# Kernel optimization log

Measured on AMD Instinct MI355X. Metric: run time of the kernel, lower is better.

## Reference

```python
import jax, jax.numpy as jnp
import numpy as np

EPS = 1e-8       # slot-attention eps
LN_EPS = 1e-5    # torch LayerNorm default
ITERS = 3        # num_iterations


def _ln(x, g, b):
    m = jnp.mean(x, axis=-1, keepdims=True)
    v = jnp.var(x, axis=-1, keepdims=True)
    return (x - m) * jax.lax.rsqrt(v + LN_EPS) * g + b


def setup_inputs() -> dict:
    key = jax.random.key(0)
    ks = jax.random.split(key, 16)
    B, N, S, D = 64, 4096, 8, 256
    s = 1.0 / np.sqrt(D)
    inp = {}
    inp["inputs"] = jax.random.normal(ks[0], (B, N, D), jnp.float32)
    inp["init_slots"] = jax.random.normal(ks[1], (B, S, D), jnp.float32)
    inp["wq"] = jax.random.normal(ks[2], (D, D), jnp.float32) * s
    inp["bq"] = jnp.zeros((D,), jnp.float32)
    inp["wk"] = jax.random.normal(ks[3], (D, D), jnp.float32) * s
    inp["bk"] = jnp.zeros((D,), jnp.float32)
    inp["wv"] = jax.random.normal(ks[4], (D, D), jnp.float32) * s
    inp["bv"] = jnp.zeros((D,), jnp.float32)
    inp["w_ih"] = jax.random.normal(ks[5], (3 * D, D), jnp.float32) * s
    inp["b_ih"] = jnp.zeros((3 * D,), jnp.float32)
    inp["w_hh"] = jax.random.normal(ks[6], (3 * D, D), jnp.float32) * s
    inp["b_hh"] = jnp.zeros((3 * D,), jnp.float32)
    inp["w1"] = jax.random.normal(ks[7], (D, D), jnp.float32) * s  # fc1_slot (hidden_dim == D)
    inp["b1"] = jnp.zeros((D,), jnp.float32)
    inp["w2"] = jax.random.normal(ks[8], (D, D), jnp.float32) * s  # fc2_slot
    inp["b2"] = jnp.zeros((D,), jnp.float32)
    inp["g_in"] = jnp.ones((D,), jnp.float32)
    inp["b_in"] = jnp.zeros((D,), jnp.float32)
    inp["g_slots"] = jnp.ones((D,), jnp.float32)
    inp["b_slots"] = jnp.zeros((D,), jnp.float32)
    inp["g_ff"] = jnp.ones((D,), jnp.float32)
    inp["b_ff"] = jnp.zeros((D,), jnp.float32)
    return inp


def reference(inputs, init_slots, wq, bq, wk, bk, wv, bv, w_ih, b_ih, w_hh, b_hh,
              w1, b1, w2, b2, g_in, b_in, g_slots, b_slots, g_ff, b_ff):
    D = inputs.shape[-1]
    scale = D ** (-0.5)
    # img_k_v: LayerNorm inputs, project to k, v
    x = _ln(inputs, g_in, b_in)
    k = x @ wk.T + bk  # [B,N,D]
    v = x @ wv.T + bv  # [B,N,D]
    slots = init_slots  # [B,S,D]
    for _ in range(ITERS):
        prev = slots
        sn = _ln(slots, g_slots, b_slots)
        q = sn @ wq.T + bq                                   # [B,S,D]
        dots = jnp.einsum('bid,bjd->bij', q, k) * scale      # [B,S,N]
        attn = jax.nn.softmax(dots, axis=1) + EPS            # softmax over slots
        attn = attn / jnp.sum(attn, axis=-1, keepdims=True)  # normalize over inputs
        updates = jnp.einsum('bjd,bij->bid', v, attn)        # [B,S,D]
        # GRUCell(updates, prev): torch gate ordering r, z, n
        gx = updates @ w_ih.T + b_ih
        gh = prev @ w_hh.T + b_hh
        xr, xz, xn = jnp.split(gx, 3, axis=-1)
        hr, hz, hn = jnp.split(gh, 3, axis=-1)
        r = jax.nn.sigmoid(xr + hr)
        z = jax.nn.sigmoid(xz + hz)
        n = jnp.tanh(xn + r * hn)
        slots = (1.0 - z) * n + z * prev
        # residual MLP
        h = jax.nn.relu(_ln(slots, g_ff, b_ff) @ w1.T + b1)
        slots = slots + h @ w2.T + b2
    return slots
```

## Files before the change

kernel.cpp:

```cpp
#include <hip/hip_runtime.h>
#include <hip/hip_bf16.h>
#include <stdint.h>

typedef unsigned short u16;
typedef __attribute__((ext_vector_type(8))) short short8;
typedef __attribute__((ext_vector_type(4))) float f32x4;

#define NB 64
#define NN 4096
#define NS 8
#define ND 256
#define NSEG 16
#define GROWS (NB*NN)

__device__ inline u16 f2bf(float f) {
    uint32_t u = __float_as_uint(f);
    u = (u + 0x7FFFu + ((u >> 16) & 1u)) >> 16;
    return (u16)u;
}
__device__ inline float bf2f(u16 h) {
    return __uint_as_float(((uint32_t)h) << 16);
}
__device__ inline f32x4 mfma16(short8 a, short8 b, f32x4 c) {
    return __builtin_amdgcn_mfma_f32_16x16x32_bf16(a, b, c, 0, 0, 0);
}
__device__ inline void gload_lds16(const u16* g, u16* l) {
    __builtin_amdgcn_global_load_lds(
        (const __attribute__((address_space(1))) void*)g,
        (__attribute__((address_space(3))) void*)l,
        16, 0, 0);
}

__global__ __launch_bounds__(256) void prep_w(
        const float* __restrict__ wv, const float* __restrict__ wk, const float* __restrict__ wq,
        const float* __restrict__ wih, const float* __restrict__ whh,
        const float* __restrict__ w1, const float* __restrict__ w2,
        u16* __restrict__ wvb, u16* __restrict__ wkTb, u16* __restrict__ wqTb,
        u16* __restrict__ wihb, u16* __restrict__ whhb,
        u16* __restrict__ w1b, u16* __restrict__ w2b) {
    int i = blockIdx.x * 256 + threadIdx.x;
    if (i < 65536) { wvb[i] = f2bf(wv[i]); return; }
    i -= 65536;
    if (i < 65536) { wkTb[i] = f2bf(wk[(i & 255)*256 + (i >> 8)]); return; }
    i -= 65536;
    if (i < 65536) { wqTb[i] = f2bf(wq[(i & 255)*256 + (i >> 8)]); return; }
    i -= 65536;
    if (i < 196608) { wihb[i] = f2bf(wih[i]); return; }
    i -= 196608;
    if (i < 196608) { whhb[i] = f2bf(whh[i]); return; }
    i -= 196608;
    if (i < 65536) { w1b[i] = f2bf(w1[i]); return; }
    i -= 65536;
    if (i < 65536) w2b[i] = f2bf(w2[i]);
}

__global__ __launch_bounds__(256) void prep_M(
        const u16* __restrict__ wkTb, const u16* __restrict__ wqTb, u16* __restrict__ Mb,
        const float* __restrict__ wq, const float* __restrict__ bk, float* __restrict__ uvec) {
    if (blockIdx.x == 16) {
        int m = threadIdx.x;
        float acc = 0.f;
        for (int o = 0; o < 256; o++) acc += wq[o*256 + m] * bk[o];
        uvec[m] = acc;
        return;
    }
    const int d0 = blockIdx.x * 16;
    const int tid = threadIdx.x, wid = tid >> 6, lane = tid & 63;
    const int l15 = lane & 15, quad = lane >> 4, kq = quad * 8;
    short8 af[8];
#pragma unroll
    for (int k = 0; k < 8; k++)
        af[k] = *reinterpret_cast<const short8*>(&wkTb[(size_t)(d0 + l15)*256 + k*32 + kq]);
#pragma unroll
    for (int ct = 0; ct < 4; ct++) {
        int m0 = (wid*4 + ct)*16;
        f32x4 a = (f32x4){0.f,0.f,0.f,0.f};
#pragma unroll
        for (int k = 0; k < 8; k++) {
            short8 bw = *reinterpret_cast<const short8*>(&wqTb[(size_t)(m0 + l15)*256 + k*32 + kq]);
            a = mfma16(af[k], bw, a);
        }
#pragma unroll
        for (int r = 0; r < 4; r++)
            Mb[(size_t)(d0 + quad*4 + r)*256 + m0 + l15] = f2bf(a[r]);
    }
}

__global__ __launch_bounds__(256) void ln_cast(
        const float* __restrict__ inp, const float* __restrict__ g,
        const float* __restrict__ bt, u16* __restrict__ xb) {
    const int tid = threadIdx.x, wid = tid >> 6, lane = tid & 63;
    const long r0 = (long)blockIdx.x * 64 + wid * 16;
    float4 g4 = reinterpret_cast<const float4*>(g)[lane];
    float4 b4 = reinterpret_cast<const float4*>(bt)[lane];
#pragma unroll 4
    for (int i = 0; i < 16; i++) {
        long row = r0 + i;
        float4 v = reinterpret_cast<const float4*>(inp + row*256)[lane];
        float s = v.x + v.y + v.z + v.w;
        float ss = v.x*v.x + v.y*v.y + v.z*v.z + v.w*v.w;
#pragma unroll
        for (int off = 32; off >= 1; off >>= 1) { s += __shfl_xor(s, off, 64); ss += __shfl_xor(ss, off, 64); }
        float mean = s * (1.0f/256.0f);
        float rstd = rsqrtf(ss * (1.0f/256.0f) - mean*mean + 1e-5f);
        ushort4 o;
        o.x = f2bf((v.x-mean)*rstd*g4.x + b4.x);
        o.y = f2bf((v.y-mean)*rstd*g4.y + b4.y);
        o.z = f2bf((v.z-mean)*rstd*g4.z + b4.z);
        o.w = f2bf((v.w-mean)*rstd*g4.w + b4.w);
        reinterpret_cast<ushort4*>(xb + row*256)[lane] = o;
    }
}

__global__ __launch_bounds__(256) void q_proj(
        const float* __restrict__ slots, const u16* __restrict__ Mb,
        const float* __restrict__ uvec,
        const float* __restrict__ gs, const float* __restrict__ bs,
        u16* __restrict__ qb, float* __restrict__ cvec) {
    __shared__ u16 sn[16*264];
    const int b = blockIdx.x;
    const int tid = threadIdx.x, wid = tid >> 6, lane = tid & 63;
    const int l15 = lane & 15, kq = (lane >> 4) * 8;
    for (int rr = wid; rr < 8; rr += 4) {
        float4 v = reinterpret_cast<const float4*>(slots + (size_t)(b*8 + rr)*256)[lane];
        float s = v.x + v.y + v.z + v.w;
        float ss = v.x*v.x + v.y*v.y + v.z*v.z + v.w*v.w;
#pragma unroll
        for (int off = 32; off >= 1; off >>= 1) { s += __shfl_xor(s, off, 64); ss += __shfl_xor(ss, off, 64); }
        float mean = s * (1.f/256.f);
        float rstd = rsqrtf(ss * (1.f/256.f) - mean*mean + 1e-5f);
        float4 g4 = reinterpret_cast<const float4*>(gs)[lane];
        float4 b4 = reinterpret_cast<const float4*>(bs)[lane];
        ushort4 o;
        o.x = f2bf((v.x-mean)*rstd*g4.x + b4.x);
        o.y = f2bf((v.y-mean)*rstd*g4.y + b4.y);
        o.z = f2bf((v.z-mean)*rstd*g4.z + b4.z);
        o.w = f2bf((v.w-mean)*rstd*g4.w + b4.w);
        *reinterpret_cast<ushort4*>(&sn[rr*264 + lane*4]) = o;
    }
    {
        ushort4 z = {0,0,0,0};
        for (int rr = 8 + wid; rr < 16; rr += 4)
            *reinterpret_cast<ushort4*>(&sn[rr*264 + lane*4]) = z;
    }
    __syncthreads();
    {
        int s = tid >> 5, l = tid & 31;
        float p = 0.f;
#pragma unroll
        for (int i = 0; i < 8; i++)
            p += bf2f(sn[s*264 + l*8 + i]) * uvec[l*8 + i];
#pragma unroll
        for (int off = 16; off >= 1; off >>= 1) p += __shfl_xor(p, off, 64);
        if (l == 0) cvec[b*8 + s] = p;
    }
    short8 af[8];
#pragma unroll
    for (int k = 0; k < 8; k++) af[k] = *reinterpret_cast<const short8*>(&sn[l15*264 + k*32 + kq]);
#pragma unroll
    for (int ct = 0; ct < 4; ct++) {
        int o0 = (wid*4 + ct)*16;
        f32x4 a = (f32x4){0.f,0.f,0.f,0.f};
#pragma unroll
        for (int k = 0; k < 8; k++) {
            short8 bw = *reinterpret_cast<const short8*>(&Mb[(size_t)(o0 + l15)*256 + k*32 + kq]);
            a = mfma16(af[k], bw, a);
        }
        if (lane < 32) {
            int sb = (lane >> 4)*4;
#pragma unroll
            for (int r = 0; r < 4; r++)
                qb[(size_t)(b*8 + sb + r)*256 + o0 + l15] = f2bf(a[r]);
        }
    }
}

__global__ __launch_bounds__(256) void attn(
        const u16* __restrict__ qt, const u16* __restrict__ xrow,
        const float* __restrict__ cvec,
        float* __restrict__ num_part, float* __restrict__ den_part) {
    __shared__ u16 xt[4][32*256];
    __shared__ u16 pb_all[4][16*36];
    __shared__ float dpd[4][8];
    const int b = blockIdx.x >> 4;
    const int seg = blockIdx.x & 15;
    const int tid = threadIdx.x, wid = tid >> 6, lane = tid & 63;
    const int l15 = lane & 15, quad = lane >> 4, kq = quad * 8;
    u16* xw = xt[wid];
    u16* pb = pb_all[wid];
    const int n_w = seg*256 + wid*64;

    {
        const int half = lane >> 5, c = lane & 31;
#pragma unroll
        for (int i = 0; i < 16; i++) {
            const int r = i*2 + half;
            const int key = (r & 7) ^ ((r >> 3) << 1);
            gload_lds16(xrow + (size_t)(b*4096 + n_w + r)*256 + (c ^ key)*8, &xw[i*2*256]);
        }
    }
#pragma unroll
    for (int k2 = 0; k2 < 9; k2++) pb[lane + k2*64] = 0;

    short8 aq[8];
    {
        const u16* qrow = &qt[((size_t)b*8 + (l15 & 7))*256 + kq];
        short8 z = {0,0,0,0,0,0,0,0};
#pragma unroll
        for (int kk = 0; kk < 8; kk++) {
            short8 t = *reinterpret_cast<const short8*>(&qrow[kk*32]);
            aq[kk] = (l15 < 8) ? t : z;
        }
    }
    float cc[4];
#pragma unroll
    for (int r = 0; r < 4; r++) {
        int rowi = quad*4 + r;
        cc[r] = (rowi < 8) ? cvec[b*8 + rowi] : 0.f;
    }
    f32x4 acc[16];
#pragma unroll
    for (int dt = 0; dt < 16; dt++) acc[dt] = (f32x4){0.f,0.f,0.f,0.f};
    float psum[4] = {0.f,0.f,0.f,0.f};

    for (int ch = 0; ch < 2; ch++) {
        const int nc = n_w + ch*32;
        const u16* kbase = &xrow[((size_t)b*4096 + nc + l15)*256 + kq];
        short8 kf[8], kn[8];
#pragma unroll
        for (int kk = 0; kk < 8; kk++) kf[kk] = *reinterpret_cast<const short8*>(&kbase[kk*32]);
#pragma unroll
        for (int nt = 0; nt < 2; nt++) {
            f32x4 dd = (f32x4){0.f,0.f,0.f,0.f};
            if (nt == 0) {
#pragma unroll
                for (int kk = 0; kk < 8; kk++) dd = mfma16(aq[kk], kf[kk], dd);
                const u16* kp = kbase + (size_t)16*256;
#pragma unroll
                for (int kk = 0; kk < 8; kk++) kn[kk] = *reinterpret_cast<const short8*>(&kp[kk*32]);
            } else {
#pragma unroll
                for (int kk = 0; kk < 8; kk++) dd = mfma16(aq[kk], kn[kk], dd);
            }
            float t0 = (dd[0] + cc[0])*0.0625f, t1 = (dd[1] + cc[1])*0.0625f;
            float t2 = (dd[2] + cc[2])*0.0625f, t3 = (dd[3] + cc[3])*0.0625f;
            float m4 = fmaxf(fmaxf(t0,t1), fmaxf(t2,t3));
            float m8 = fmaxf(m4, __shfl_xor(m4, 16, 64));
            float e0 = __expf(t0-m8), e1 = __expf(t1-m8), e2 = __expf(t2-m8), e3 = __expf(t3-m8);
            float s4 = e0+e1+e2+e3;
            float s8 = s4 + __shfl_xor(s4, 16, 64);
            float inv = 1.0f / s8;
            u16 h0 = f2bf(e0*inv + 1e-8f);
            u16 h1 = f2bf(e1*inv + 1e-8f);
            u16 h2 = f2bf(e2*inv + 1e-8f);
            u16 h3 = f2bf(e3*inv + 1e-8f);
            if (lane < 32) {
                int sb = quad*4, col = nt*16 + l15;
                pb[(sb+0)*36 + col] = h0;
                pb[(sb+1)*36 + col] = h1;
                pb[(sb+2)*36 + col] = h2;
                pb[(sb+3)*36 + col] = h3;
                psum[0] += bf2f(h0); psum[1] += bf2f(h1);
                psum[2] += bf2f(h2); psum[3] += bf2f(h3);
            }
        }
        __builtin_amdgcn_s_waitcnt(0x0070);
        __builtin_amdgcn_sched_barrier(0);
        short8 ap = *reinterpret_cast<const short8*>(&pb[l15*36 + kq]);
        const int d = l15;
#pragma unroll
        for (int dt = 0; dt < 16; dt++) {
            const int dd2 = dt*16 + d;
            const int d3 = dd2 >> 3, d7 = dd2 & 7;
            const int rowb = quad*8*256 + d7;
            const int c3 = d3 ^ (quad << 1);
            short8 pv;
#pragma unroll
            for (int j = 0; j < 8; j++)
                pv[j] = (short)xw[rowb + j*256 + ((c3 ^ j) << 3)];
            acc[dt] = mfma16(ap, pv, acc[dt]);
        }
        if (ch == 0) {
            const int half = lane >> 5, c = lane & 31;
#pragma unroll
            for (int i = 0; i < 16; i++) {
                const int r = i*2 + half;
                const int key = (r & 7) ^ ((r >> 3) << 1);
                gload_lds16(xrow + (size_t)(b*4096 + n_w + 32 + r)*256 + (c ^ key)*8, &xw[i*2*256]);
            }
        }
    }
#pragma unroll
    for (int off = 1; off < 16; off <<= 1) {
#pragma unroll
        for (int r = 0; r < 4; r++) psum[r] += __shfl_xor(psum[r], off, 64);
    }
    if (quad < 2 && l15 == 0) {
#pragma unroll
        for (int r = 0; r < 4; r++) dpd[wid][quad*4 + r] = psum[r];
    }
    float* rw = (float*)&xt[wid][0];
    if (lane < 32) {
        int sb = quad*4;
#pragma unroll
        for (int dt = 0; dt < 16; dt++) {
            int d0 = dt*16 + l15;
#pragma unroll
            for (int r = 0; r < 4; r++)
                rw[(sb+r)*256 + d0] = acc[dt][r];
        }
    }
    __syncthreads();
    const float* F = (const float*)&xt[0][0];
    for (int idx = tid; idx < 2048; idx += 256) {
        float v = F[idx] + F[4096 + idx] + F[8192 + idx] + F[12288 + idx];
        num_part[((size_t)(b*16 + seg))*2048 + idx] = v;
    }
    if (tid < 8)
        den_part[(b*16 + seg)*8 + tid] = dpd[0][tid] + dpd[1][tid] + dpd[2][tid] + dpd[3][tid];
}

__global__ __launch_bounds__(768) void finalize(
        const float* __restrict__ slots_in, const float* __restrict__ num_part, const float* __restrict__ den_part,
        const u16* __restrict__ wihb, const float* __restrict__ bih,
        const u16* __restrict__ whhb, const float* __restrict__ bhh,
        const u16* __restrict__ w1b, const float* __restrict__ b1v,
        const u16* __restrict__ w2b, const float* __restrict__ b2v,
        const u16* __restrict__ wvb, const float* __restrict__ bvv,
        const float* __restrict__ gff, const float* __restrict__ bff,
        float* __restrict__ slots_out,
        const u16* __restrict__ Mb, const float* __restrict__ uvec,
        const float* __restrict__ gs, const float* __restrict__ bs,
        u16* __restrict__ qb, float* __restrict__ cvec, int do_q) {
    __shared__ u16 updb[16*264];
    __shared__ u16 prevb[16*264];
    __shared__ u16 lnb[16*264];
    __shared__ float gx[8*776];
    __shared__ float gh[8*776];
    __shared__ float snew[8*256];
    __shared__ float dsum_s[8];
    float* sfin = gx;
    const int b = blockIdx.x;
    const int tid = threadIdx.x, wid = tid >> 6, lane = tid & 63;
    const int l15 = lane & 15, kq = (lane >> 4) * 8;
    if (tid < 8) {
        float ds = 0.f;
#pragma unroll
        for (int sg = 0; sg < 16; sg++) ds += den_part[(b*16 + sg)*8 + tid];
        dsum_s[tid] = ds;
    }
    __syncthreads();
    for (int idx = tid; idx < 2048; idx += 768) {
        int s = idx >> 8, d = idx & 255;
        float ns = 0.f;
#pragma unroll
        for (int sg = 0; sg < 16; sg++)
            ns += num_part[((size_t)(b*16 + sg)*8 + s)*256 + d];
        updb[s*264 + d] = f2bf(ns / dsum_s[s]);
        prevb[s*264 + d] = f2bf(slots_in[(size_t)(b*8 + s)*256 + d]);
        updb[(8+s)*264 + d] = 0;
        prevb[(8+s)*264 + d] = 0;
        lnb[(8+s)*264 + d] = 0;
    }
    __syncthreads();
    {
        short8 av[8];
#pragma unroll
        for (int k = 0; k < 8; k++)
            av[k] = *reinterpret_cast<const short8*>(&updb[l15*264 + k*32 + kq]);
        for (int ct = wid; ct < 16; ct += 12) {
            int o0 = ct*16;
            f32x4 a = (f32x4){0.f,0.f,0.f,0.f};
#pragma unroll
            for (int k = 0; k < 8; k++) {
                short8 bw = *reinterpret_cast<const short8*>(&wvb[(size_t)(o0 + l15)*256 + k*32 + kq]);
                a = mfma16(av[k], bw, a);
            }
            if (lane < 32) {
                int sb = (lane >> 4)*4, o = o0 + l15;
                float bb2 = bvv[o];
#pragma unroll
                for (int r = 0; r < 4; r++)
                    lnb[(sb+r)*264 + o] = f2bf(a[r] + bb2);
            }
        }
    }
    __syncthreads();
    short8 au[8], ap[8];
#pragma unroll
    for (int k = 0; k < 8; k++) {
        au[k] = *reinterpret_cast<const short8*>(&lnb[l15*264 + k*32 + kq]);
        ap[k] = *reinterpret_cast<const short8*>(&prevb[l15*264 + k*32 + kq]);
    }
#pragma unroll
    for (int ct = 0; ct < 4; ct++) {
        int o0 = (wid*4 + ct)*16;
        f32x4 ax = (f32x4){0.f,0.f,0.f,0.f}, ah = (f32x4){0.f,0.f,0.f,0.f};
#pragma unroll
        for (int k = 0; k < 8; k++) {
            short8 bx = *reinterpret_cast<const short8*>(&wihb[(size_t)(o0 + l15)*256 + k*32 + kq]);
            short8 bh = *reinterpret_cast<const short8*>(&whhb[(size_t)(o0 + l15)*256 + k*32 + kq]);
            ax = mfma16(au[k], bx, ax);
            ah = mfma16(ap[k], bh, ah);
        }
        if (lane < 32) {
            int sb = (lane >> 4)*4, o = o0 + l15;
            float bxs = bih[o], bhs = bhh[o];
#pragma unroll
            for (int r = 0; r < 4; r++) {
                gx[(sb+r)*776 + o] = ax[r] + bxs;
                gh[(sb+r)*776 + o] = ah[r] + bhs;
            }
        }
    }
    __syncthreads();
    for (int idx = tid; idx < 2048; idx += 768) {
        int s = idx >> 8, j = idx & 255;
        float xr = gx[s*776 + j], xz = gx[s*776 + 256 + j], xn = gx[s*776 + 512 + j];
        float hr = gh[s*776 + j], hz = gh[s*776 + 256 + j], hn = gh[s*776 + 512 + j];
        float r_ = 1.f/(1.f + __expf(-(xr+hr)));
        float z_ = 1.f/(1.f + __expf(-(xz+hz)));
        float n_ = tanhf(xn + r_*hn);
        float pv = slots_in[(size_t)(b*8 + s)*256 + j];
        snew[s*256 + j] = (1.f - z_)*n_ + z_*pv;
    }
    __syncthreads();
    if (wid < 8) {
        int rr = wid;
        float4 v = reinterpret_cast<const float4*>(&snew[rr*256])[lane];
        float s = v.x + v.y + v.z + v.w;
        float ss = v.x*v.x + v.y*v.y + v.z*v.z + v.w*v.w;
#pragma unroll
        for (int off = 32; off >= 1; off >>= 1) { s += __shfl_xor(s, off, 64); ss += __shfl_xor(ss, off, 64); }
        float mean = s * (1.f/256.f);
        float rstd = rsqrtf(ss * (1.f/256.f) - mean*mean + 1e-5f);
        float4 g4 = reinterpret_cast<const float4*>(gff)[lane];
        float4 b4 = reinterpret_cast<const float4*>(bff)[lane];
        ushort4 o;
        o.x = f2bf((v.x-mean)*rstd*g4.x + b4.x);
        o.y = f2bf((v.y-mean)*rstd*g4.y + b4.y);
        o.z = f2bf((v.z-mean)*rstd*g4.z + b4.z);
        o.w = f2bf((v.w-mean)*rstd*g4.w + b4.w);
        *reinterpret_cast<ushort4*>(&lnb[rr*264 + lane*4]) = o;
    } else {
        ushort4 z = {0,0,0,0};
        *reinterpret_cast<ushort4*>(&lnb[wid*264 + lane*4]) = z;
        *reinterpret_cast<ushort4*>(&lnb[(wid+4)*264 + lane*4]) = z;
    }
    __syncthreads();
    short8 al[8];
#pragma unroll
    for (int k = 0; k < 8; k++) al[k] = *reinterpret_cast<const short8*>(&lnb[l15*264 + k*32 + kq]);
    for (int ct = wid; ct < 16; ct += 12) {
        int o0 = ct*16;
        f32x4 a = (f32x4){0.f,0.f,0.f,0.f};
#pragma unroll
        for (int k = 0; k < 8; k++) {
            short8 bw = *reinterpret_cast<const short8*>(&w1b[(size_t)(o0 + l15)*256 + k*32 + kq]);
            a = mfma16(al[k], bw, a);
        }
        if (lane < 32) {
            int sb = (lane >> 4)*4, o = o0 + l15;
            float bb = b1v[o];
#pragma unroll
            for (int r = 0; r < 4; r++)
                updb[(sb+r)*264 + o] = f2bf(fmaxf(a[r] + bb, 0.f));
        }
    }
    __syncthreads();
    short8 ah2[8];
#pragma unroll
    for (int k = 0; k < 8; k++) ah2[k] = *reinterpret_cast<const short8*>(&updb[l15*264 + k*32 + kq]);
    for (int ct = wid; ct < 16; ct += 12) {
        int o0 = ct*16;
        f32x4 a = (f32x4){0.f,0.f,0.f,0.f};
#pragma unroll
        for (int k = 0; k < 8; k++) {
            short8 bw = *reinterpret_cast<const short8*>(&w2b[(size_t)(o0 + l15)*256 + k*32 + kq]);
            a = mfma16(ah2[k], bw, a);
        }
        if (lane < 32) {
            int sb = (lane >> 4)*4, o = o0 + l15;
            float bb = b2v[o];
#pragma unroll
            for (int r = 0; r < 4; r++) {
                float vfin = snew[(sb+r)*256 + o] + a[r] + bb;
                slots_out[(size_t)(b*8 + sb + r)*256 + o] = vfin;
                sfin[(sb+r)*256 + o] = vfin;
            }
        }
    }
    if (!do_q) return;
    __syncthreads();
    if (wid < 8) {
        int rr = wid;
        float4 v = reinterpret_cast<const float4*>(&sfin[rr*256])[lane];
        float s = v.x + v.y + v.z + v.w;
        float ss = v.x*v.x + v.y*v.y + v.z*v.z + v.w*v.w;
#pragma unroll
        for (int off = 32; off >= 1; off >>= 1) { s += __shfl_xor(s, off, 64); ss += __shfl_xor(ss, off, 64); }
        float mean = s * (1.f/256.f);
        float rstd = rsqrtf(ss * (1.f/256.f) - mean*mean + 1e-5f);
        float4 g4 = reinterpret_cast<const float4*>(gs)[lane];
        float4 b4 = reinterpret_cast<const float4*>(bs)[lane];
        ushort4 o;
        o.x = f2bf((v.x-mean)*rstd*g4.x + b4.x);
        o.y = f2bf((v.y-mean)*rstd*g4.y + b4.y);
        o.z = f2bf((v.z-mean)*rstd*g4.z + b4.z);
        o.w = f2bf((v.w-mean)*rstd*g4.w + b4.w);
        *reinterpret_cast<ushort4*>(&lnb[rr*264 + lane*4]) = o;
    } else {
        ushort4 z = {0,0,0,0};
        *reinterpret_cast<ushort4*>(&lnb[wid*264 + lane*4]) = z;
        *reinterpret_cast<ushort4*>(&lnb[(wid+4)*264 + lane*4]) = z;
    }
    __syncthreads();
    if (tid < 256) {
        int s = tid >> 5, l = tid & 31;
        float p = 0.f;
#pragma unroll
        for (int i = 0; i < 8; i++)
            p += bf2f(lnb[s*264 + l*8 + i]) * uvec[l*8 + i];
#pragma unroll
        for (int off = 16; off >= 1; off >>= 1) p += __shfl_xor(p, off, 64);
        if (l == 0) cvec[b*8 + s] = p;
    }
    short8 alq[8];
#pragma unroll
    for (int k = 0; k < 8; k++) alq[k] = *reinterpret_cast<const short8*>(&lnb[l15*264 + k*32 + kq]);
    for (int ct = wid; ct < 16; ct += 12) {
        int o0 = ct*16;
        f32x4 a = (f32x4){0.f,0.f,0.f,0.f};
#pragma unroll
        for (int k = 0; k < 8; k++) {
            short8 bw = *reinterpret_cast<const short8*>(&Mb[(size_t)(o0 + l15)*256 + k*32 + kq]);
            a = mfma16(alq[k], bw, a);
        }
        if (lane < 32) {
            int sb = (lane >> 4)*4, o = o0 + l15;
#pragma unroll
            for (int r = 0; r < 4; r++)
                qb[(size_t)(b*8 + sb + r)*256 + o] = f2bf(a[r]);
        }
    }
}

extern "C" void kernel_launch(void* const* d_in, const int* in_sizes, int n_in,
                              void* d_out, int out_size, void* d_ws, size_t ws_size,
                              hipStream_t stream) {
    (void)in_sizes; (void)n_in; (void)out_size;
    const float* inputs     = (const float*)d_in[0];
    const float* init_slots = (const float*)d_in[1];
    const float* wq  = (const float*)d_in[2];
    const float* bq  = (const float*)d_in[3];  (void)bq;
    const float* wk  = (const float*)d_in[4];
    const float* bk  = (const float*)d_in[5];
    const float* wv  = (const float*)d_in[6];
    const float* bv  = (const float*)d_in[7];
    const float* wih = (const float*)d_in[8];
    const float* bih = (const float*)d_in[9];
    const float* whh = (const float*)d_in[10];
    const float* bhh = (const float*)d_in[11];
    const float* w1  = (const float*)d_in[12];
    const float* b1  = (const float*)d_in[13];
    const float* w2  = (const float*)d_in[14];
    const float* b2  = (const float*)d_in[15];
    const float* g_in = (const float*)d_in[16];
    const float* b_in = (const float*)d_in[17];
    const float* g_sl = (const float*)d_in[18];
    const float* b_sl = (const float*)d_in[19];
    const float* g_ff = (const float*)d_in[20];
    const float* b_ff = (const float*)d_in[21];

    char* ws = (char*)d_ws;
    size_t off = 0;
    auto alloc = [&](size_t bytes) -> void* {
        void* p = ws + off;
        off += (bytes + 255) & ~(size_t)255;
        return p;
    };
    u16* xb    = (u16*)alloc((size_t)GROWS * ND * 2);
    u16* qbf   = (u16*)alloc((size_t)NB * NS * ND * 2);
    float* slots = (float*)alloc((size_t)NB * NS * ND * 4);
    float* nump  = (float*)alloc((size_t)NB * NSEG * NS * ND * 4);
    float* denp  = (float*)alloc((size_t)NB * NSEG * NS * 4);
    float* cvec  = (float*)alloc((size_t)NB * NS * 4);
    float* uvec  = (float*)alloc(256 * 4);
    u16* wvb  = (u16*)alloc(65536 * 2);
    u16* wkTb = (u16*)alloc(65536 * 2);
    u16* wqTb = (u16*)alloc(65536 * 2);
    u16* Mb   = (u16*)alloc(65536 * 2);
    u16* wihb = (u16*)alloc(196608 * 2);
    u16* whhb = (u16*)alloc(196608 * 2);
    u16* w1b  = (u16*)alloc(65536 * 2);
    u16* w2b  = (u16*)alloc(65536 * 2);
    if (off > ws_size) return;

    prep_w<<<2816, 256, 0, stream>>>(wv, wk, wq, wih, whh, w1, w2,
                                     wvb, wkTb, wqTb, wihb, whhb, w1b, w2b);
    prep_M<<<17, 256, 0, stream>>>(wkTb, wqTb, Mb, wq, bk, uvec);
    hipMemcpyAsync(slots, init_slots, (size_t)NB * NS * ND * 4,
                   hipMemcpyDeviceToDevice, stream);
    ln_cast<<<GROWS / 64, 256, 0, stream>>>(inputs, g_in, b_in, xb);
    q_proj<<<NB, 256, 0, stream>>>(slots, Mb, uvec, g_sl, b_sl, qbf, cvec);
    for (int it = 0; it < 3; it++) {
        attn<<<NB * 16, 256, 0, stream>>>(qbf, xb, cvec, nump, denp);
        float* outp = (it == 2) ? (float*)d_out : slots;
        finalize<<<NB, 768, 0, stream>>>(slots, nump, denp, wihb, bih, whhb, bhh,
                                         w1b, b1, w2b, b2, wvb, bv, g_ff, b_ff, outp,
                                         Mb, uvec, g_sl, b_sl, qbf, cvec, (it < 2) ? 1 : 0);
    }
}
```

Baseline: 719.4 us.

## Restructure attn kernel into block-wide double-buffered 64-row tiles split by D

```diff
diff --git a/kernel.cpp b/kernel.cpp
--- a/kernel.cpp
+++ b/kernel.cpp
@@ -10,7 +10,7 @@
 #define NN 4096
 #define NS 8
 #define ND 256
-#define NSEG 16
+#define NSEG 8
 #define GROWS (NB*NN)
 
 __device__ inline u16 f2bf(float f) {
@@ -179,29 +179,34 @@
         const u16* __restrict__ qt, const u16* __restrict__ xrow,
         const float* __restrict__ cvec,
         float* __restrict__ num_part, float* __restrict__ den_part) {
-    __shared__ u16 xt[4][32*256];
-    __shared__ u16 pb_all[4][16*36];
+    __shared__ u16 xt[2][64*256];
+    __shared__ u16 pt[16*72];
     __shared__ float dpd[4][8];
-    const int b = blockIdx.x >> 4;
-    const int seg = blockIdx.x & 15;
+    const int b = blockIdx.x >> 3;
+    const int seg = blockIdx.x & 7;
     const int tid = threadIdx.x, wid = tid >> 6, lane = tid & 63;
     const int l15 = lane & 15, quad = lane >> 4, kq = quad * 8;
-    u16* xw = xt[wid];
-    u16* pb = pb_all[wid];
-    const int n_w = seg*256 + wid*64;
-
+    const int n0 = seg * 512;
+    const u16* xsrc = xrow + (size_t)b*4096*256;
+
+    auto STAGE = [&](int t) {
+        u16* dst = &xt[t & 1][(wid*16) * 256];
+        const u16* src = xsrc + (size_t)(n0 + t*64 + wid*16) * 256;
+        const int half = lane >> 5, c = lane & 31;
+#pragma unroll
+        for (int i = 0; i < 8; i++) {
+            const int rl = wid*16 + i*2 + half;
+            const int key = (rl & 7) ^ ((rl >> 3) & 7);
+            gload_lds16(src + (size_t)(i*2 + half)*256 + ((c ^ key))*8, dst + i*2*256);
+        }
+    };
+
+    STAGE(0);
     {
-        const int half = lane >> 5, c = lane & 31;
-#pragma unroll
-        for (int i = 0; i < 16; i++) {
-            const int r = i*2 + half;
-            const int key = (r & 7) ^ ((r >> 3) << 1);
-            gload_lds16(xrow + (size_t)(b*4096 + n_w + r)*256 + (c ^ key)*8, &xw[i*2*256]);
-        }
-    }
-#pragma unroll
-    for (int k2 = 0; k2 < 9; k2++) pb[lane + k2*64] = 0;
-
+        ushort4 z4 = {0,0,0,0};
+        if (tid < 144)
+            *reinterpret_cast<ushort4*>(&pt[8*72 + tid*4]) = z4;
+    }
     short8 aq[8];
     {
         const u16* qrow = &qt[((size_t)b*8 + (l15 & 7))*256 + kq];
@@ -218,77 +223,67 @@
         int rowi = quad*4 + r;
         cc[r] = (rowi < 8) ? cvec[b*8 + rowi] : 0.f;
     }
-    f32x4 acc[16];
-#pragma unroll
-    for (int dt = 0; dt < 16; dt++) acc[dt] = (f32x4){0.f,0.f,0.f,0.f};
+    f32x4 acc[4];
+#pragma unroll
+    for (int dt = 0; dt < 4; dt++) acc[dt] = (f32x4){0.f,0.f,0.f,0.f};
     float psum[4] = {0.f,0.f,0.f,0.f};
 
-    for (int ch = 0; ch < 2; ch++) {
-        const int nc = n_w + ch*32;
-        const u16* kbase = &xrow[((size_t)b*4096 + nc + l15)*256 + kq];
-        short8 kf[8], kn[8];
-#pragma unroll
-        for (int kk = 0; kk < 8; kk++) kf[kk] = *reinterpret_cast<const short8*>(&kbase[kk*32]);
-#pragma unroll
-        for (int nt = 0; nt < 2; nt++) {
-            f32x4 dd = (f32x4){0.f,0.f,0.f,0.f};
-            if (nt == 0) {
-#pragma unroll
-                for (int kk = 0; kk < 8; kk++) dd = mfma16(aq[kk], kf[kk], dd);
-                const u16* kp = kbase + (size_t)16*256;
-#pragma unroll
-                for (int kk = 0; kk < 8; kk++) kn[kk] = *reinterpret_cast<const short8*>(&kp[kk*32]);
-            } else {
-#pragma unroll
-                for (int kk = 0; kk < 8; kk++) dd = mfma16(aq[kk], kn[kk], dd);
+    __syncthreads();
+
+    for (int t = 0; t < 8; t++) {
+        if (t < 7) STAGE(t + 1);
+        const u16* tw = xt[t & 1];
+        const int rq = wid*16 + l15;
+        const int keyq = (rq & 7) ^ ((rq >> 3) & 7);
+        f32x4 dd = (f32x4){0.f,0.f,0.f,0.f};
+#pragma unroll
+        for (int kk = 0; kk < 8; kk++) {
+            short8 bf = *reinterpret_cast<const short8*>(
+                &tw[rq*256 + (((kk*4 + quad) ^ keyq))*8]);
+            dd = mfma16(aq[kk], bf, dd);
+        }
+        float t0 = (dd[0] + cc[0])*0.0625f, t1 = (dd[1] + cc[1])*0.0625f;
+        float t2 = (dd[2] + cc[2])*0.0625f, t3 = (dd[3] + cc[3])*0.0625f;
+        float m4 = fmaxf(fmaxf(t0,t1), fmaxf(t2,t3));
+        float m8 = fmaxf(m4, __shfl_xor(m4, 16, 64));
+        float e0 = __expf(t0-m8), e1 = __expf(t1-m8), e2 = __expf(t2-m8), e3 = __expf(t3-m8);
+        float s4 = e0+e1+e2+e3;
+        float s8 = s4 + __shfl_xor(s4, 16, 64);
+        float inv = 1.0f / s8;
+        u16 h0 = f2bf(e0*inv + 1e-8f);
+        u16 h1 = f2bf(e1*inv + 1e-8f);
+        u16 h2 = f2bf(e2*inv + 1e-8f);
+        u16 h3 = f2bf(e3*inv + 1e-8f);
+        if (lane < 32) {
+            int sb = quad*4, col = wid*16 + l15;
+            pt[(sb+0)*72 + col] = h0;
+            pt[(sb+1)*72 + col] = h1;
+            pt[(sb+2)*72 + col] = h2;
+            pt[(sb+3)*72 + col] = h3;
+            psum[0] += bf2f(h0); psum[1] += bf2f(h1);
+            psum[2] += bf2f(h2); psum[3] += bf2f(h3);
+        }
+        __syncthreads();
+        short8 ap0 = *reinterpret_cast<const short8*>(&pt[l15*72 + kq]);
+        short8 ap1 = *reinterpret_cast<const short8*>(&pt[l15*72 + 32 + kq]);
+#pragma unroll
+        for (int dt = 0; dt < 4; dt++) {
+            const int d = (wid*4 + dt)*16 + l15;
+            const int g = d >> 3, e = d & 7;
+            short8 pv0, pv1;
+#pragma unroll
+            for (int j = 0; j < 8; j++) {
+                const int ra = quad*8 + j;
+                const int ka = (ra & 7) ^ ((ra >> 3) & 7);
+                pv0[j] = (short)tw[ra*256 + ((g ^ ka))*8 + e];
+                const int rb2 = 32 + quad*8 + j;
+                const int kb2 = (rb2 & 7) ^ ((rb2 >> 3) & 7);
+                pv1[j] = (short)tw[rb2*256 + ((g ^ kb2))*8 + e];
             }
-            float t0 = (dd[0] + cc[0])*0.0625f, t1 = (dd[1] + cc[1])*0.0625f;
-            float t2 = (dd[2] + cc[2])*0.0625f, t3 = (dd[3] + cc[3])*0.0625f;
-            float m4 = fmaxf(fmaxf(t0,t1), fmaxf(t2,t3));
-            float m8 = fmaxf(m4, __shfl_xor(m4, 16, 64));
-            float e0 = __expf(t0-m8), e1 = __expf(t1-m8), e2 = __expf(t2-m8), e3 = __expf(t3-m8);
-            float s4 = e0+e1+e2+e3;
-            float s8 = s4 + __shfl_xor(s4, 16, 64);
-            float inv = 1.0f / s8;
-            u16 h0 = f2bf(e0*inv + 1e-8f);
-            u16 h1 = f2bf(e1*inv + 1e-8f);
-            u16 h2 = f2bf(e2*inv + 1e-8f);
-            u16 h3 = f2bf(e3*inv + 1e-8f);
-            if (lane < 32) {
-                int sb = quad*4, col = nt*16 + l15;
-                pb[(sb+0)*36 + col] = h0;
-                pb[(sb+1)*36 + col] = h1;
-                pb[(sb+2)*36 + col] = h2;
-                pb[(sb+3)*36 + col] = h3;
-                psum[0] += bf2f(h0); psum[1] += bf2f(h1);
-                psum[2] += bf2f(h2); psum[3] += bf2f(h3);
-            }
-        }
-        __builtin_amdgcn_s_waitcnt(0x0070);
-        __builtin_amdgcn_sched_barrier(0);
-        short8 ap = *reinterpret_cast<const short8*>(&pb[l15*36 + kq]);
-        const int d = l15;
-#pragma unroll
-        for (int dt = 0; dt < 16; dt++) {
-            const int dd2 = dt*16 + d;
-            const int d3 = dd2 >> 3, d7 = dd2 & 7;
-            const int rowb = quad*8*256 + d7;
-            const int c3 = d3 ^ (quad << 1);
-            short8 pv;
-#pragma unroll
-            for (int j = 0; j < 8; j++)
-                pv[j] = (short)xw[rowb + j*256 + ((c3 ^ j) << 3)];
-            acc[dt] = mfma16(ap, pv, acc[dt]);
-        }
-        if (ch == 0) {
-            const int half = lane >> 5, c = lane & 31;
-#pragma unroll
-            for (int i = 0; i < 16; i++) {
-                const int r = i*2 + half;
-                const int key = (r & 7) ^ ((r >> 3) << 1);
-                gload_lds16(xrow + (size_t)(b*4096 + n_w + 32 + r)*256 + (c ^ key)*8, &xw[i*2*256]);
-            }
-        }
+            acc[dt] = mfma16(ap0, pv0, acc[dt]);
+            acc[dt] = mfma16(ap1, pv1, acc[dt]);
+        }
+        __syncthreads();
     }
 #pragma unroll
     for (int off = 1; off < 16; off <<= 1) {
@@ -299,25 +294,17 @@
 #pragma unroll
         for (int r = 0; r < 4; r++) dpd[wid][quad*4 + r] = psum[r];
     }
-    float* rw = (float*)&xt[wid][0];
-    if (lane < 32) {
-        int sb = quad*4;
-#pragma unroll
-        for (int dt = 0; dt < 16; dt++) {
-            int d0 = dt*16 + l15;
-#pragma unroll
-            for (int r = 0; r < 4; r++)
-                rw[(sb+r)*256 + d0] = acc[dt][r];
-        }
-    }
-    __syncthreads();
-    const float* F = (const float*)&xt[0][0];
-    for (int idx = tid; idx < 2048; idx += 256) {
-        float v = F[idx] + F[4096 + idx] + F[8192 + idx] + F[12288 + idx];
-        num_part[((size_t)(b*16 + seg))*2048 + idx] = v;
-    }
+    const size_t base = (size_t)(b*8 + seg) * 8;
+    if (quad < 2) {
+#pragma unroll
+        for (int dt = 0; dt < 4; dt++)
+#pragma unroll
+            for (int rr = 0; rr < 4; rr++)
+                num_part[(base + quad*4 + rr)*256 + (wid*4 + dt)*16 + l15] = acc[dt][rr];
+    }
+    __syncthreads();
     if (tid < 8)
-        den_part[(b*16 + seg)*8 + tid] = dpd[0][tid] + dpd[1][tid] + dpd[2][tid] + dpd[3][tid];
+        den_part[base + tid] = dpd[0][tid] + dpd[1][tid] + dpd[2][tid] + dpd[3][tid];
 }
 
 __global__ __launch_bounds__(768) void finalize(
@@ -346,7 +333,7 @@
     if (tid < 8) {
         float ds = 0.f;
 #pragma unroll
-        for (int sg = 0; sg < 16; sg++) ds += den_part[(b*16 + sg)*8 + tid];
+        for (int sg = 0; sg < NSEG; sg++) ds += den_part[(b*NSEG + sg)*8 + tid];
         dsum_s[tid] = ds;
     }
     __syncthreads();
@@ -354,8 +341,8 @@
         int s = idx >> 8, d = idx & 255;
         float ns = 0.f;
 #pragma unroll
-        for (int sg = 0; sg < 16; sg++)
-            ns += num_part[((size_t)(b*16 + sg)*8 + s)*256 + d];
+        for (int sg = 0; sg < NSEG; sg++)
+            ns += num_part[((size_t)(b*NSEG + sg)*8 + s)*256 + d];
         updb[s*264 + d] = f2bf(ns / dsum_s[s]);
         prevb[s*264 + d] = f2bf(slots_in[(size_t)(b*8 + s)*256 + d]);
         updb[(8+s)*264 + d] = 0;
@@ -604,7 +591,7 @@
     ln_cast<<<GROWS / 64, 256, 0, stream>>>(inputs, g_in, b_in, xb);
     q_proj<<<NB, 256, 0, stream>>>(slots, Mb, uvec, g_sl, b_sl, qbf, cvec);
     for (int it = 0; it < 3; it++) {
-        attn<<<NB * 16, 256, 0, stream>>>(qbf, xb, cvec, nump, denp);
+        attn<<<NB * NSEG, 256, 0, stream>>>(qbf, xb, cvec, nump, denp);
         float* outp = (it == 2) ? (float*)d_out : slots;
         finalize<<<NB, 768, 0, stream>>>(slots, nump, denp, wihb, bih, whhb, bhh,
                                          w1b, b1, w2b, b2, wvb, bv, g_ff, b_ff, outp,
```

New measurement: 646.0 us. 10.2% less time.
